# Kernel tuning notes

Measured on AMD Instinct MI355X. Metric: run time of the kernel, lower is better.

Reference implementation:

```python
import jax, jax.numpy as jnp
import numpy as np

D = 256        # d_model
NH = 8         # num_head
NL = 4         # num_level
KS = 8         # kernel_size (even)
K2 = KS * KS
HD = D // NH   # head_dim
LEVELS = [(128, 128), (64, 64), (32, 32), (16, 16)]


def _kernel_indices():
    # even kernel: linspace(-KS/2+0.5, KS/2-0.5, KS), meshgrid ij, stack [j,i] (x,y), / KS
    idx = np.linspace(-KS // 2 + 0.5, KS // 2 - 0.5, KS).astype(np.float32)
    i, j = np.meshgrid(idx, idx, indexing='ij')
    return jnp.asarray(np.stack([j, i], axis=-1).reshape(-1, 2) / KS)  # [K2, 2]


def setup_inputs():
    key = jax.random.key(0)
    ks = jax.random.split(key, 12)
    b, q = 2, 300
    l2 = sum(h * w for h, w in LEVELS)
    query = jax.random.normal(ks[0], (b, q, D), jnp.float32)
    value = jax.random.normal(ks[1], (b, l2, D), jnp.float32)
    v_shape = np.array(LEVELS, dtype=np.int64)                      # [NL, 2] (H, W)
    starts = np.concatenate([[0], np.cumsum([h * w for h, w in LEVELS])[:-1]])
    v_start_index = starts.astype(np.int64)                          # [NL]
    v_mask = jnp.zeros((b, l2), dtype=bool)                          # no padding
    v_valid_ratios = jnp.ones((b, 1, 1, NL, 1, 2), jnp.float32)
    center = jax.random.uniform(ks[2], (b, q, 2), jnp.float32, 0.25, 0.75)
    size = jax.random.uniform(ks[3], (b, q, 2), jnp.float32, 0.05, 0.25)
    ref_windows = jnp.concatenate([center, size], axis=-1)           # [b, q, 4] cx,cy,w,h
    s = 0.02
    Wv = s * jax.random.normal(ks[4], (D, D), jnp.float32)
    bv = jnp.zeros((D,), jnp.float32)
    Wbox = s * jax.random.normal(ks[5], (NH * NL * 4, D), jnp.float32)
    bbox = jax.random.uniform(ks[6], (NH * NL * 4,), jnp.float32)    # uniform init per _reset_parameters
    Wattn = s * jax.random.normal(ks[7], (NH * NL * 4, D), jnp.float32)
    battn = s * jax.random.normal(ks[8], (NH * NL * 4,), jnp.float32)
    Wout = s * jax.random.normal(ks[9], (D, D), jnp.float32)
    bout = jnp.zeros((D,), jnp.float32)
    return dict(query=query, value=value, v_shape=v_shape, v_mask=v_mask,
                v_start_index=v_start_index, v_valid_ratios=v_valid_ratios,
                ref_windows=ref_windows, Wv=Wv, bv=bv, Wbox=Wbox, bbox=bbox,
                Wattn=Wattn, battn=battn, Wout=Wout, bout=bout,
                kernel_indices=_kernel_indices())


def reference(query, value, v_shape, v_mask, v_start_index, v_valid_ratios,
              ref_windows, Wv, bv, Wbox, bbox, Wattn, battn, Wout, bout,
              kernel_indices):
    b, q, _ = query.shape
    # value projection + mask fill
    val = jnp.einsum('bnd,ed->bne', value, Wv) + bv
    val = jnp.where(v_mask[..., None], 0.0, val)
    val = val.reshape(b, -1, NH, HD)                                 # [b, l2, NH, HD]

    # attention logits: base 2x2 grid expanded to KSxKS via repeat_interleave
    aw = (jnp.einsum('bqd,od->bqo', query, Wattn) + battn).reshape(b, q, NH, NL, 2, 2)
    aw = jnp.repeat(jnp.repeat(aw, KS // 2, axis=-1), KS // 2, axis=-2)  # [b,q,NH,NL,KS,KS]
    spatial = jax.nn.softmax(aw.reshape(b, q, NH, NL * K2), axis=-1).reshape(b, q, NH, NL, K2)
    level = jax.nn.softmax(aw, axis=3).reshape(b, q, NH, NL, K2)

    # sampling grid (_where_to_attend)
    ob = (jnp.einsum('bqd,od->bqo', query, Wbox) + bbox).reshape(b, q, NH, NL, 4)
    rw = ref_windows[:, :, None, None, :]                            # [b,q,1,1,4]
    boxes = rw + ob / 8.0 * rw[..., jnp.array([2, 3, 2, 3])]
    center = boxes[..., None, :2]                                    # [b,q,NH,NL,1,2]
    size = boxes[..., None, 2:]
    grid = center + kernel_indices * jax.nn.relu(size)               # [b,q,NH,NL,K2,2]
    grid = grid * v_valid_ratios

    # multi-level bilinear sampling (grid_sample, align_corners=False, zero padding)
    bi = jnp.arange(b)[:, None, None, None]
    hi = jnp.arange(NH)[None, None, :, None]
    sampled = []
    for lv in range(NL):
        Hl = int(v_shape[lv, 0]); Wl = int(v_shape[lv, 1]); st = int(v_start_index[lv])
        vl = val[:, st:st + Hl * Wl]                                 # [b, Hl*Wl, NH, HD]
        loc = grid[:, :, :, lv]                                      # [b,q,NH,K2,2]
        x = loc[..., 0] * Wl - 0.5
        y = loc[..., 1] * Hl - 0.5
        x0 = jnp.floor(x); y0 = jnp.floor(y)
        dx = x - x0; dy = y - y0
        acc = jnp.zeros((b, q, NH, K2, HD), val.dtype)
        for ix, iy, w in ((x0, y0, (1 - dx) * (1 - dy)),
                          (x0 + 1, y0, dx * (1 - dy)),
                          (x0, y0 + 1, (1 - dx) * dy),
                          (x0 + 1, y0 + 1, dx * dy)):
            valid = (ix >= 0) & (ix < Wl) & (iy >= 0) & (iy < Hl)
            idx = (jnp.clip(iy, 0, Hl - 1) * Wl + jnp.clip(ix, 0, Wl - 1)).astype(jnp.int32)
            v4 = vl[bi, idx, hi]                                     # [b,q,NH,K2,HD]
            acc = acc + jnp.where(valid, w, 0.0)[..., None] * v4
        sampled.append(acc)
    sampled = jnp.stack(sampled, axis=3)                             # [b,q,NH,NL,K2,HD]

    # box-attention output: spatial softmax over all (level, point)
    out = jnp.einsum('bqhlkd,bqhlk->bqhd', sampled, spatial).reshape(b, q, D)
    out = jnp.einsum('bqd,od->bqo', out, Wout) + bout
    # instance mask output: level softmax per kernel point
    mask = jnp.einsum('bqhlkd,bqhlk->bqkhd', sampled, level).reshape(b, q, K2, D)
    mask = jnp.einsum('bqkd,od->bqko', mask, Wout) + bout
    return out, mask
```

## Files before the change

### kernel.cpp

```cpp
#include <hip/hip_runtime.h>
#include <cstdint>
#include <cstddef>

typedef unsigned short u16;
typedef unsigned int   u32;
typedef __attribute__((ext_vector_type(8))) short bf16x8;
typedef __attribute__((ext_vector_type(4))) float f32x4;

static constexpr int kQ = 300;
static constexpr int kL2 = 21760;

__device__ __forceinline__ u16 bf16_rne(float f) {
    u32 u = __float_as_uint(f);
    u += 0x7FFFu + ((u >> 16) & 1u);
    return (u16)(u >> 16);
}
__device__ __forceinline__ u32 pack2(float lo, float hi) {
    return (u32)bf16_rne(lo) | ((u32)bf16_rne(hi) << 16);
}
__device__ __forceinline__ float lo16(u32 u) { return __uint_as_float(u << 16); }
__device__ __forceinline__ float hi16(u32 u) { return __uint_as_float(u & 0xFFFF0000u); }

#define GLOAD(kt) { \
    const int k0 = (kt) * 32; \
    if constexpr (A_F32) { \
        const float* p = (const float*)Aptr + (size_t)(m0 + arow) * 256 + k0 + asub * 8; \
        ra0 = *(const float4*)p; ra1 = *(const float4*)(p + 4); \
    } else { \
        rav = *(const uint4*)((const u16*)Aptr + (size_t)(m0 + arow) * 256 + k0 + asub * 8); \
    } \
    rb0 = *(const uint4*)(W + (size_t)(n0 + b0row) * 256 + k0 + bsub * 8); \
    rb1 = *(const uint4*)(W + (size_t)(n0 + b1row) * 256 + k0 + bsub * 8); }

#define GSTORE(buf) { \
    u16* As = S + (buf) * 6144; \
    u16* Bs = As + 2048; \
    const int ac = asub * 64 + ((arow + 2 * asub) & 63); \
    if constexpr (A_F32) { \
        uint4 o; \
        o.x = pack2(ra0.x, ra0.y); o.y = pack2(ra0.z, ra0.w); \
        o.z = pack2(ra1.x, ra1.y); o.w = pack2(ra1.z, ra1.w); \
        *(uint4*)(As + (ac << 3)) = o; \
    } else { \
        *(uint4*)(As + (ac << 3)) = rav; \
    } \
    *(uint4*)(Bs + ((bsub * 128 + ((b0row + 2 * bsub) & 127)) << 3)) = rb0; \
    *(uint4*)(Bs + ((bsub * 128 + ((b1row + 2 * bsub) & 127)) << 3)) = rb1; }

template<bool A_F32, bool OUT_BF16>
__global__ __launch_bounds__(256)
void gemm_bf16(const void* __restrict__ Aptr, const u16* __restrict__ W,
               const float* __restrict__ bias, void* __restrict__ Cout,
               const unsigned char* __restrict__ rowmask)
{
    __shared__ u16 S[12288];
    const int tid = threadIdx.x;
    const int m0 = blockIdx.x * 64;
    const int n0 = blockIdx.y * 128;
    const int lane = tid & 63;
    const int w = tid >> 6;
    const int wm = w & 1, wn = w >> 1;
    const int g = lane >> 4, r = lane & 15;

    const int arow = tid >> 2, asub = tid & 3;
    const int b0row = tid >> 2;
    const int b1row = 64 + (tid >> 2);
    const int bsub = tid & 3;

    f32x4 acc[2][4];
#pragma unroll
    for (int i = 0; i < 2; i++)
#pragma unroll
        for (int j = 0; j < 4; j++)
            acc[i][j] = (f32x4){0.f, 0.f, 0.f, 0.f};

    float4 ra0, ra1; uint4 rav; uint4 rb0, rb1;

    GLOAD(0);
    GSTORE(0);
    for (int kt = 0; kt < 8; ++kt) {
        if (kt < 7) GLOAD(kt + 1);
        __syncthreads();
        const u16* As = S + (kt & 1) * 6144;
        const u16* Bs = As + 2048;
        bf16x8 af[2], bf[4];
#pragma unroll
        for (int mf = 0; mf < 2; ++mf) {
            int X = wm * 32 + mf * 16 + r;
            af[mf] = *(const bf16x8*)(As + ((g * 64 + ((X + 2 * g) & 63)) << 3));
        }
#pragma unroll
        for (int nf = 0; nf < 4; ++nf) {
            int X = wn * 64 + nf * 16 + r;
            bf[nf] = *(const bf16x8*)(Bs + ((g * 128 + ((X + 2 * g) & 127)) << 3));
        }
#pragma unroll
        for (int mf = 0; mf < 2; ++mf)
#pragma unroll
            for (int nf = 0; nf < 4; ++nf)
                acc[mf][nf] = __builtin_amdgcn_mfma_f32_16x16x32_bf16(
                    af[mf], bf[nf], acc[mf][nf], 0, 0, 0);
        if (kt < 7) GSTORE((kt + 1) & 1);
    }

    if constexpr (!OUT_BF16) {
        float* C = (float*)Cout;
#pragma unroll
        for (int nf = 0; nf < 4; ++nf) {
            int ng = n0 + wn * 64 + nf * 16 + r;
            float bb = bias[ng];
#pragma unroll
            for (int mf = 0; mf < 2; ++mf) {
                int mg = m0 + wm * 32 + mf * 16 + g * 4;
#pragma unroll
                for (int reg = 0; reg < 4; ++reg) {
                    float z = 1.f;
                    if (rowmask && rowmask[mg + reg]) z = 0.f;
                    C[(size_t)(mg + reg) * 256 + ng] = (acc[mf][nf][reg] + bb) * z;
                }
            }
        }
    } else {
        u16* C = (u16*)Cout;
#pragma unroll
        for (int round = 0; round < 2; ++round) {
            __syncthreads();
            if (wn == round) {
#pragma unroll
                for (int nf = 0; nf < 4; ++nf) {
                    int col = nf * 16 + r;
                    float bb = bias[n0 + round * 64 + col];
#pragma unroll
                    for (int mf = 0; mf < 2; ++mf) {
                        int row0 = wm * 32 + mf * 16 + g * 4;
#pragma unroll
                        for (int reg = 0; reg < 4; ++reg) {
                            float z = 1.f;
                            if (rowmask && rowmask[m0 + row0 + reg]) z = 0.f;
                            S[(row0 + reg) * 64 + col] =
                                bf16_rne((acc[mf][nf][reg] + bb) * z);
                        }
                    }
                }
            }
            __syncthreads();
#pragma unroll
            for (int i = 0; i < 2; ++i) {
                int c = tid + i * 256;
                int row = c >> 3, cc = c & 7;
                *(uint4*)(C + (size_t)(m0 + row) * 256 + n0 + round * 64 + cc * 8) =
                    *(const uint4*)(S + row * 64 + cc * 8);
            }
        }
    }
}

__global__ __launch_bounds__(256)
void gemm_out_fused(const float* __restrict__ out_part, const float* __restrict__ W,
                    const float* __restrict__ bias, float* __restrict__ C, int M)
{
    __shared__ float As[32][68];
    __shared__ float Ws[32][68];
    const int tid = threadIdx.x;
    const int m0 = blockIdx.x * 64;
    const int n0 = blockIdx.y * 64;
    const int tx = tid & 15, ty = tid >> 4;
    const size_t KQS = (size_t)600 * 256;
    float acc[4][4] = {};

    for (int k0 = 0; k0 < 256; k0 += 32) {
#pragma unroll
        for (int i = 0; i < 2; i++) {
            int t = tid + i * 256;
            int rr = t >> 3;
            int c4 = (t & 7) << 2;
            int ra = min(m0 + rr, M - 1);
            const float* p = out_part + (size_t)ra * 256 + k0 + c4;
            float4 v0 = *(const float4*)p;
            float4 v1 = *(const float4*)(p + KQS);
            float4 v2 = *(const float4*)(p + 2 * KQS);
            float4 v3 = *(const float4*)(p + 3 * KQS);
            float4 va;
            va.x = (v0.x + v1.x) + (v2.x + v3.x);
            va.y = (v0.y + v1.y) + (v2.y + v3.y);
            va.z = (v0.z + v1.z) + (v2.z + v3.z);
            va.w = (v0.w + v1.w) + (v2.w + v3.w);
            As[c4 + 0][rr] = va.x; As[c4 + 1][rr] = va.y;
            As[c4 + 2][rr] = va.z; As[c4 + 3][rr] = va.w;
            float4 vw = *(const float4*)(W + (size_t)(n0 + rr) * 256 + k0 + c4);
            Ws[c4 + 0][rr] = vw.x; Ws[c4 + 1][rr] = vw.y;
            Ws[c4 + 2][rr] = vw.z; Ws[c4 + 3][rr] = vw.w;
        }
        __syncthreads();
#pragma unroll
        for (int kk = 0; kk < 32; kk++) {
            float4 a = *(const float4*)&As[kk][ty * 4];
            float4 wv4 = *(const float4*)&Ws[kk][tx * 4];
            float av[4] = {a.x, a.y, a.z, a.w};
            float wv[4] = {wv4.x, wv4.y, wv4.z, wv4.w};
#pragma unroll
            for (int i = 0; i < 4; i++)
#pragma unroll
                for (int j = 0; j < 4; j++)
                    acc[i][j] += av[i] * wv[j];
        }
        __syncthreads();
    }
#pragma unroll
    for (int i = 0; i < 4; i++) {
        int rr = m0 + ty * 4 + i;
        if (rr >= M) continue;
        int n = n0 + tx * 4;
        float4 o;
        o.x = acc[i][0] + bias[n + 0];
        o.y = acc[i][1] + bias[n + 1];
        o.z = acc[i][2] + bias[n + 2];
        o.w = acc[i][3] + bias[n + 3];
        *(float4*)(C + (size_t)rr * 256 + n) = o;
    }
}

__global__ __launch_bounds__(256)
void prep_kernel(const float* __restrict__ Wv, u16* __restrict__ Wv_b,
                 const float* __restrict__ Wout, u16* __restrict__ Wout_b,
                 const float* __restrict__ query,
                 const float* __restrict__ Wattn, const float* __restrict__ battn,
                 const float* __restrict__ Wbox,  const float* __restrict__ bbox,
                 const float* __restrict__ ref_windows,
                 const float* __restrict__ vvr,
                 float* __restrict__ params)
{
    if (blockIdx.x < 64) {
        const float* src = (blockIdx.x < 32) ? Wv : Wout;
        u16* dst = (blockIdx.x < 32) ? Wv_b : Wout_b;
        int i = ((blockIdx.x & 31) * 256 + threadIdx.x) * 8;
        float4 a = *(const float4*)(src + i);
        float4 b = *(const float4*)(src + i + 4);
        uint4 o;
        o.x = pack2(a.x, a.y); o.y = pack2(a.z, a.w);
        o.z = pack2(b.x, b.y); o.w = pack2(b.z, b.w);
        *(uint4*)(dst + i) = o;
        return;
    }

    __shared__ float qrow[256];
    __shared__ float awob[256];
    __shared__ float4 boxs[8][4];
    __shared__ float wgts[8][4][4];
    __shared__ float cqds[8][4];

    const int bq = blockIdx.x - 64;
    const int b = bq / kQ;
    const int tid = threadIdx.x;

    if (tid < 64)
        ((float4*)qrow)[tid] = ((const float4*)(query + (size_t)bq * 256))[tid];
    __syncthreads();

    {
        const float* Wrow = (tid < 128) ? (Wattn + (size_t)tid * 256)
                                        : (Wbox + (size_t)(tid - 128) * 256);
        float s = (tid < 128) ? battn[tid] : bbox[tid - 128];
#pragma unroll 8
        for (int d4 = 0; d4 < 64; d4++) {
            float4 wv = ((const float4*)Wrow)[d4];
            float4 qv = ((const float4*)qrow)[d4];
            s += wv.x * qv.x + wv.y * qv.y + wv.z * qv.z + wv.w * qv.w;
        }
        awob[tid] = s;
    }
    __syncthreads();

    if (tid < 8) {
        const int h = tid;
        float m = -1e30f;
        float E[16];
#pragma unroll
        for (int i = 0; i < 16; i++) m = fmaxf(m, awob[h * 16 + i]);
        float Ssum = 0.f;
#pragma unroll
        for (int i = 0; i < 16; i++) { E[i] = expf(awob[h * 16 + i] - m); Ssum += E[i]; }
        float invS16 = 1.f / (16.f * Ssum);
#pragma unroll
        for (int qd = 0; qd < 4; qd++) {
            float Sq = E[qd] + E[4 + qd] + E[8 + qd] + E[12 + qd];
            float inv = 1.f / Sq;
#pragma unroll
            for (int l = 0; l < 4; l++) wgts[h][l][qd] = E[l * 4 + qd] * inv;
            cqds[h][qd] = Sq * invS16;
        }
    }
    if (tid >= 64 && tid < 96) {
        const int t = tid - 64;
        const int h = t >> 2, l = t & 3;
        float4 rw = ((const float4*)ref_windows)[bq];
        float ob0 = awob[128 + h * 16 + l * 4 + 0];
        float ob1 = awob[128 + h * 16 + l * 4 + 1];
        float ob2 = awob[128 + h * 16 + l * 4 + 2];
        float ob3 = awob[128 + h * 16 + l * 4 + 3];
        float cx = rw.x + ob0 * 0.125f * rw.z;
        float cy = rw.y + ob1 * 0.125f * rw.w;
        float sx = fmaxf(rw.z + ob2 * 0.125f * rw.z, 0.f);
        float sy = fmaxf(rw.w + ob3 * 0.125f * rw.w, 0.f);
        float vrx = vvr[(b * 4 + l) * 2 + 0];
        float vry = vvr[(b * 4 + l) * 2 + 1];
        boxs[h][l] = make_float4(cx * vrx, cy * vry, sx * vrx, sy * vry);
    }
    __syncthreads();

    float* p = params + (size_t)bq * 288;
    if (tid < 32)       ((float4*)p)[tid] = ((float4*)boxs)[tid];
    else if (tid < 64)  ((float4*)p)[tid] = ((float4*)wgts)[tid - 32];
    else if (tid < 72)  ((float4*)p)[tid] = ((float4*)cqds)[tid - 64];
}

__global__ __launch_bounds__(512)
void sample_bf16(const u16* __restrict__ valb,
                 const float* __restrict__ params,
                 u16* __restrict__ maskb,
                 float* __restrict__ out_part)
{
    __shared__ float4 boxs[8][4];
    __shared__ float wgts[8][4][4];
    __shared__ float cqds[8][4];
    __shared__ float warr[8][256];

    const int blk = blockIdx.x;
    const int bq = blk % 600;
    const int kq = blk / 600;
    const int b = bq / kQ;
    const int tid = threadIdx.x;

    if (tid < 72) {
        float4 v = ((const float4*)(params + (size_t)bq * 288))[tid];
        if (tid < 32)      ((float4*)boxs)[tid] = v;
        else if (tid < 64) ((float4*)wgts)[tid - 32] = v;
        else               ((float4*)cqds)[tid - 64] = v;
    }
    __syncthreads();

    const int klocal = tid >> 5;
    const int h = (tid >> 2) & 7;
    const int ch = tid & 3;
    const int k = kq * 16 + klocal;
    const float kx = (float)(k & 7) * 0.125f - 0.4375f;
    const float ky = (float)(k >> 3) * 0.125f - 0.4375f;
    const int qd = (((k >> 5) & 1) << 1) | ((k >> 2) & 1);

    float acc[8];
#pragma unroll
    for (int e = 0; e < 8; e++) acc[e] = 0.f;

    static constexpr int LW[4]  = {128, 64, 32, 16};
    static constexpr int LST[4] = {0, 16384, 20480, 21504};

#pragma unroll
    for (int l = 0; l < 4; l++) {
        const int Wl = LW[l];
        const u16* vbase = valb + ((size_t)(b * kL2 + LST[l]) << 8) + h * 32 + ch * 8;
        float4 bx = boxs[h][l];
        float lw = wgts[h][l][qd];
        float x = (bx.x + kx * bx.z) * Wl - 0.5f;
        float y = (bx.y + ky * bx.w) * Wl - 0.5f;
        float x0f = floorf(x), y0f = floorf(y);
        float dx = x - x0f, dy = y - y0f;
        int x0 = (int)x0f, y0 = (int)y0f;
        int x1 = x0 + 1, y1 = y0 + 1;
        int x0c = min(max(x0, 0), Wl - 1), x1c = min(max(x1, 0), Wl - 1);
        int y0c = min(max(y0, 0), Wl - 1), y1c = min(max(y1, 0), Wl - 1);
        float vx0 = (x0 >= 0 && x0 < Wl) ? 1.f : 0.f;
        float vx1 = (x1 >= 0 && x1 < Wl) ? 1.f : 0.f;
        float vy0 = (y0 >= 0 && y0 < Wl) ? 1.f : 0.f;
        float vy1 = (y1 >= 0 && y1 < Wl) ? 1.f : 0.f;
        float w00 = (1.f - dx) * (1.f - dy) * vx0 * vy0 * lw;
        float w10 = dx * (1.f - dy) * vx1 * vy0 * lw;
        float w01 = (1.f - dx) * dy * vx0 * vy1 * lw;
        float w11 = dx * dy * vx1 * vy1 * lw;
        uint4 v00 = *(const uint4*)(vbase + ((size_t)(y0c * Wl + x0c) << 8));
        uint4 v10 = *(const uint4*)(vbase + ((size_t)(y0c * Wl + x1c) << 8));
        uint4 v01 = *(const uint4*)(vbase + ((size_t)(y1c * Wl + x0c) << 8));
        uint4 v11 = *(const uint4*)(vbase + ((size_t)(y1c * Wl + x1c) << 8));
        acc[0] += w00*lo16(v00.x) + w10*lo16(v10.x) + w01*lo16(v01.x) + w11*lo16(v11.x);
        acc[1] += w00*hi16(v00.x) + w10*hi16(v10.x) + w01*hi16(v01.x) + w11*hi16(v11.x);
        acc[2] += w00*lo16(v00.y) + w10*lo16(v10.y) + w01*lo16(v01.y) + w11*lo16(v11.y);
        acc[3] += w00*hi16(v00.y) + w10*hi16(v10.y) + w01*hi16(v01.y) + w11*hi16(v11.y);
        acc[4] += w00*lo16(v00.z) + w10*lo16(v10.z) + w01*lo16(v01.z) + w11*lo16(v11.z);
        acc[5] += w00*hi16(v00.z) + w10*hi16(v10.z) + w01*hi16(v01.z) + w11*hi16(v11.z);
        acc[6] += w00*lo16(v00.w) + w10*lo16(v10.w) + w01*lo16(v01.w) + w11*lo16(v11.w);
        acc[7] += w00*hi16(v00.w) + w10*hi16(v10.w) + w01*hi16(v01.w) + w11*hi16(v11.w);
    }

    {
        uint4 o;
        o.x = pack2(acc[0], acc[1]);
        o.y = pack2(acc[2], acc[3]);
        o.z = pack2(acc[4], acc[5]);
        o.w = pack2(acc[6], acc[7]);
        *(uint4*)(maskb + (((size_t)bq * 64 + k) << 8) + h * 32 + ch * 8) = o;
    }

    {
        const int wave = tid >> 6;
        const int lane = tid & 63;
        float c = cqds[h][qd];
#pragma unroll
        for (int e = 0; e < 8; e++) {
            float v = acc[e] * c;
            v += __shfl_xor(v, 32);
            if (lane < 32) warr[wave][h * 32 + ch * 8 + e] = v;
        }
    }
    __syncthreads();
    if (tid < 256) {
        float s = 0.f;
#pragma unroll
        for (int wv = 0; wv < 8; wv++) s += warr[wv][tid];
        out_part[(size_t)blk * 256 + tid] = s;
    }
}

extern "C" void kernel_launch(void* const* d_in, const int* in_sizes, int n_in,
                              void* d_out, int out_size, void* d_ws, size_t ws_size,
                              hipStream_t stream)
{
    const float* query       = (const float*)d_in[0];
    const float* value       = (const float*)d_in[1];
    const unsigned char* v_mask = (const unsigned char*)d_in[3];
    const float* vvr         = (const float*)d_in[5];
    const float* ref_windows = (const float*)d_in[6];
    const float* Wv    = (const float*)d_in[7];
    const float* bv    = (const float*)d_in[8];
    const float* Wbox  = (const float*)d_in[9];
    const float* bbox  = (const float*)d_in[10];
    const float* Wattn = (const float*)d_in[11];
    const float* battn = (const float*)d_in[12];
    const float* Wout  = (const float*)d_in[13];
    const float* bout  = (const float*)d_in[14];

    char* wsp = (char*)d_ws;
    u16* Wv_b    = (u16*)wsp;                 wsp += (size_t)65536 * 2;
    u16* Wout_b  = (u16*)wsp;                 wsp += (size_t)65536 * 2;
    u16* val_b   = (u16*)wsp;                 wsp += (size_t)11141120 * 2;
    u16* mask_b  = (u16*)wsp;                 wsp += (size_t)9830400 * 2;
    float* params   = (float*)wsp;            wsp += (size_t)600 * 288 * 4;
    float* out_part = (float*)wsp;            wsp += (size_t)2400 * 256 * 4;

    float* out  = (float*)d_out;
    float* mask = out + (size_t)600 * 256;

    prep_kernel<<<664, 256, 0, stream>>>(Wv, Wv_b, Wout, Wout_b,
                                         query, Wattn, battn, Wbox, bbox,
                                         ref_windows, vvr, params);
    gemm_bf16<true, true><<<dim3(680, 2), 256, 0, stream>>>(value, Wv_b, bv, val_b, v_mask);
    sample_bf16<<<2400, 512, 0, stream>>>(val_b, params, mask_b, out_part);
    gemm_bf16<false, false><<<dim3(600, 2), 256, 0, stream>>>(mask_b, Wout_b, bout, mask, nullptr);
    gemm_out_fused<<<dim3(10, 4), 256, 0, stream>>>(out_part, Wout, bout, out, 600);
}
```

Baseline: 127.3 us.

## Process two kernel points per thread in sampler and merge output GEMM into mask GEMM

Each sampling thread now handles two horizontally adjacent kernel points. They share the y interpolation and row bases, which halves the sampler grid and the number of partial-output slices. The small fp32 output projection no longer has its own launch: it runs as 20 extra blocks of the mask GEMM grid, and it sums two partial slices instead of four. Occupancy hints are also added to the sampler. The intent is to cut launch overhead and redundant coordinate math, at the cost of more registers per thread and fewer sampler blocks.

```diff
diff --git a/kernel.cpp b/kernel.cpp
--- a/kernel.cpp
+++ b/kernel.cpp
@@ -47,14 +47,79 @@
     *(uint4*)(Bs + ((bsub * 128 + ((b0row + 2 * bsub) & 127)) << 3)) = rb0; \
     *(uint4*)(Bs + ((bsub * 128 + ((b1row + 2 * bsub) & 127)) << 3)) = rb1; }
 
-template<bool A_F32, bool OUT_BF16>
+template<bool A_F32, bool OUT_BF16, bool MERGED_OUT>
 __global__ __launch_bounds__(256)
 void gemm_bf16(const void* __restrict__ Aptr, const u16* __restrict__ W,
                const float* __restrict__ bias, void* __restrict__ Cout,
-               const unsigned char* __restrict__ rowmask)
+               const unsigned char* __restrict__ rowmask,
+               const float* __restrict__ Wf,
+               const float* __restrict__ opart,
+               float* __restrict__ C2)
 {
     __shared__ u16 S[12288];
     const int tid = threadIdx.x;
+
+    if constexpr (MERGED_OUT) {
+        if (blockIdx.x >= 600) {
+            float (*As2)[68] = reinterpret_cast<float(*)[68]>(S);
+            float (*Ws2)[68] = reinterpret_cast<float(*)[68]>((char*)S + 8704);
+            const int t20 = blockIdx.x - 600;
+            const int m0o = (t20 % 10) * 64;
+            const int nq  = (t20 / 10) * 2 + blockIdx.y;
+            const int n0o = nq * 64;
+            const int tx = tid & 15, ty = tid >> 4;
+            const size_t KQS = (size_t)600 * 256;
+            float acc[4][4] = {};
+            for (int k0 = 0; k0 < 256; k0 += 32) {
+#pragma unroll
+                for (int i = 0; i < 2; i++) {
+                    int t = tid + i * 256;
+                    int rr = t >> 3;
+                    int c4 = (t & 7) << 2;
+                    int ra = min(m0o + rr, 599);
+                    const float* p = opart + (size_t)ra * 256 + k0 + c4;
+                    float4 v0 = *(const float4*)p;
+                    float4 v1 = *(const float4*)(p + KQS);
+                    float4 va;
+                    va.x = v0.x + v1.x; va.y = v0.y + v1.y;
+                    va.z = v0.z + v1.z; va.w = v0.w + v1.w;
+                    As2[c4 + 0][rr] = va.x; As2[c4 + 1][rr] = va.y;
+                    As2[c4 + 2][rr] = va.z; As2[c4 + 3][rr] = va.w;
+                    float4 vw = *(const float4*)(Wf + (size_t)(n0o + rr) * 256 + k0 + c4);
+                    Ws2[c4 + 0][rr] = vw.x; Ws2[c4 + 1][rr] = vw.y;
+                    Ws2[c4 + 2][rr] = vw.z; Ws2[c4 + 3][rr] = vw.w;
+                }
+                __syncthreads();
+#pragma unroll
+                for (int kk = 0; kk < 32; kk++) {
+                    float4 a = *(const float4*)&As2[kk][ty * 4];
+                    float4 wv4 = *(const float4*)&Ws2[kk][tx * 4];
+                    float av[4] = {a.x, a.y, a.z, a.w};
+                    float wv[4] = {wv4.x, wv4.y, wv4.z, wv4.w};
+#pragma unroll
+                    for (int i = 0; i < 4; i++)
+#pragma unroll
+                        for (int jj = 0; jj < 4; jj++)
+                            acc[i][jj] += av[i] * wv[jj];
+                }
+                __syncthreads();
+            }
+#pragma unroll
+            for (int i = 0; i < 4; i++) {
+                int rr = m0o + ty * 4 + i;
+                if (rr >= 600) continue;
+                int n = n0o + tx * 4;
+                float4 o;
+                o.x = acc[i][0] + bias[n + 0];
+                o.y = acc[i][1] + bias[n + 1];
+                o.z = acc[i][2] + bias[n + 2];
+                o.w = acc[i][3] + bias[n + 3];
+                *(float4*)(C2 + (size_t)rr * 256 + n) = o;
+            }
+            return;
+        }
+    }
+
     const int m0 = blockIdx.x * 64;
     const int n0 = blockIdx.y * 128;
     const int lane = tid & 63;
@@ -152,71 +217,6 @@
                     *(const uint4*)(S + row * 64 + cc * 8);
             }
         }
-    }
-}
-
-__global__ __launch_bounds__(256)
-void gemm_out_fused(const float* __restrict__ out_part, const float* __restrict__ W,
-                    const float* __restrict__ bias, float* __restrict__ C, int M)
-{
-    __shared__ float As[32][68];
-    __shared__ float Ws[32][68];
-    const int tid = threadIdx.x;
-    const int m0 = blockIdx.x * 64;
-    const int n0 = blockIdx.y * 64;
-    const int tx = tid & 15, ty = tid >> 4;
-    const size_t KQS = (size_t)600 * 256;
-    float acc[4][4] = {};
-
-    for (int k0 = 0; k0 < 256; k0 += 32) {
-#pragma unroll
-        for (int i = 0; i < 2; i++) {
-            int t = tid + i * 256;
-            int rr = t >> 3;
-            int c4 = (t & 7) << 2;
-            int ra = min(m0 + rr, M - 1);
-            const float* p = out_part + (size_t)ra * 256 + k0 + c4;
-            float4 v0 = *(const float4*)p;
-            float4 v1 = *(const float4*)(p + KQS);
-            float4 v2 = *(const float4*)(p + 2 * KQS);
-            float4 v3 = *(const float4*)(p + 3 * KQS);
-            float4 va;
-            va.x = (v0.x + v1.x) + (v2.x + v3.x);
-            va.y = (v0.y + v1.y) + (v2.y + v3.y);
-            va.z = (v0.z + v1.z) + (v2.z + v3.z);
-            va.w = (v0.w + v1.w) + (v2.w + v3.w);
-            As[c4 + 0][rr] = va.x; As[c4 + 1][rr] = va.y;
-            As[c4 + 2][rr] = va.z; As[c4 + 3][rr] = va.w;
-            float4 vw = *(const float4*)(W + (size_t)(n0 + rr) * 256 + k0 + c4);
-            Ws[c4 + 0][rr] = vw.x; Ws[c4 + 1][rr] = vw.y;
-            Ws[c4 + 2][rr] = vw.z; Ws[c4 + 3][rr] = vw.w;
-        }
-        __syncthreads();
-#pragma unroll
-        for (int kk = 0; kk < 32; kk++) {
-            float4 a = *(const float4*)&As[kk][ty * 4];
-            float4 wv4 = *(const float4*)&Ws[kk][tx * 4];
-            float av[4] = {a.x, a.y, a.z, a.w};
-            float wv[4] = {wv4.x, wv4.y, wv4.z, wv4.w};
-#pragma unroll
-            for (int i = 0; i < 4; i++)
-#pragma unroll
-                for (int j = 0; j < 4; j++)
-                    acc[i][j] += av[i] * wv[j];
-        }
-        __syncthreads();
-    }
-#pragma unroll
-    for (int i = 0; i < 4; i++) {
-        int rr = m0 + ty * 4 + i;
-        if (rr >= M) continue;
-        int n = n0 + tx * 4;
-        float4 o;
-        o.x = acc[i][0] + bias[n + 0];
-        o.y = acc[i][1] + bias[n + 1];
-        o.z = acc[i][2] + bias[n + 2];
-        o.w = acc[i][3] + bias[n + 3];
-        *(float4*)(C + (size_t)rr * 256 + n) = o;
     }
 }
 
@@ -314,7 +314,7 @@
     else if (tid < 72)  ((float4*)p)[tid] = ((float4*)cqds)[tid - 64];
 }
 
-__global__ __launch_bounds__(512)
+__global__ __launch_bounds__(512, 4)
 void sample_bf16(const u16* __restrict__ valb,
                  const float* __restrict__ params,
                  u16* __restrict__ maskb,
@@ -327,7 +327,7 @@
 
     const int blk = blockIdx.x;
     const int bq = blk % 600;
-    const int kq = blk / 600;
+    const int kh = blk / 600;
     const int b = bq / kQ;
     const int tid = threadIdx.x;
 
@@ -339,17 +339,19 @@
     }
     __syncthreads();
 
-    const int klocal = tid >> 5;
+    const int j = tid >> 5;
     const int h = (tid >> 2) & 7;
     const int ch = tid & 3;
-    const int k = kq * 16 + klocal;
-    const float kx = (float)(k & 7) * 0.125f - 0.4375f;
-    const float ky = (float)(k >> 3) * 0.125f - 0.4375f;
-    const int qd = (((k >> 5) & 1) << 1) | ((k >> 2) & 1);
-
-    float acc[8];
-#pragma unroll
-    for (int e = 0; e < 8; e++) acc[e] = 0.f;
+    const int J = kh * 16 + j;
+    const int ka = 2 * J;
+    const float kxa = (float)(ka & 7) * 0.125f - 0.4375f;
+    const float kxb = kxa + 0.125f;
+    const float ky  = (float)(ka >> 3) * 0.125f - 0.4375f;
+    const int qd = (((ka >> 5) & 1) << 1) | ((ka >> 2) & 1);
+
+    float acca[8], accb[8];
+#pragma unroll
+    for (int e = 0; e < 8; e++) { acca[e] = 0.f; accb[e] = 0.f; }
 
     static constexpr int LW[4]  = {128, 64, 32, 16};
     static constexpr int LST[4] = {0, 16384, 20480, 21504};
@@ -360,43 +362,56 @@
         const u16* vbase = valb + ((size_t)(b * kL2 + LST[l]) << 8) + h * 32 + ch * 8;
         float4 bx = boxs[h][l];
         float lw = wgts[h][l][qd];
-        float x = (bx.x + kx * bx.z) * Wl - 0.5f;
         float y = (bx.y + ky * bx.w) * Wl - 0.5f;
-        float x0f = floorf(x), y0f = floorf(y);
-        float dx = x - x0f, dy = y - y0f;
-        int x0 = (int)x0f, y0 = (int)y0f;
-        int x1 = x0 + 1, y1 = y0 + 1;
-        int x0c = min(max(x0, 0), Wl - 1), x1c = min(max(x1, 0), Wl - 1);
+        float y0f = floorf(y);
+        float dy = y - y0f;
+        int y0 = (int)y0f, y1 = y0 + 1;
         int y0c = min(max(y0, 0), Wl - 1), y1c = min(max(y1, 0), Wl - 1);
-        float vx0 = (x0 >= 0 && x0 < Wl) ? 1.f : 0.f;
-        float vx1 = (x1 >= 0 && x1 < Wl) ? 1.f : 0.f;
         float vy0 = (y0 >= 0 && y0 < Wl) ? 1.f : 0.f;
         float vy1 = (y1 >= 0 && y1 < Wl) ? 1.f : 0.f;
-        float w00 = (1.f - dx) * (1.f - dy) * vx0 * vy0 * lw;
-        float w10 = dx * (1.f - dy) * vx1 * vy0 * lw;
-        float w01 = (1.f - dx) * dy * vx0 * vy1 * lw;
-        float w11 = dx * dy * vx1 * vy1 * lw;
-        uint4 v00 = *(const uint4*)(vbase + ((size_t)(y0c * Wl + x0c) << 8));
-        uint4 v10 = *(const uint4*)(vbase + ((size_t)(y0c * Wl + x1c) << 8));
-        uint4 v01 = *(const uint4*)(vbase + ((size_t)(y1c * Wl + x0c) << 8));
-        uint4 v11 = *(const uint4*)(vbase + ((size_t)(y1c * Wl + x1c) << 8));
-        acc[0] += w00*lo16(v00.x) + w10*lo16(v10.x) + w01*lo16(v01.x) + w11*lo16(v11.x);
-        acc[1] += w00*hi16(v00.x) + w10*hi16(v10.x) + w01*hi16(v01.x) + w11*hi16(v11.x);
-        acc[2] += w00*lo16(v00.y) + w10*lo16(v10.y) + w01*lo16(v01.y) + w11*lo16(v11.y);
-        acc[3] += w00*hi16(v00.y) + w10*hi16(v10.y) + w01*hi16(v01.y) + w11*hi16(v11.y);
-        acc[4] += w00*lo16(v00.z) + w10*lo16(v10.z) + w01*lo16(v01.z) + w11*lo16(v11.z);
-        acc[5] += w00*hi16(v00.z) + w10*hi16(v10.z) + w01*hi16(v01.z) + w11*hi16(v11.z);
-        acc[6] += w00*lo16(v00.w) + w10*lo16(v10.w) + w01*lo16(v01.w) + w11*lo16(v11.w);
-        acc[7] += w00*hi16(v00.w) + w10*hi16(v10.w) + w01*hi16(v01.w) + w11*hi16(v11.w);
+        float wy0 = (1.f - dy) * vy0 * lw;
+        float wy1 = dy * vy1 * lw;
+        const u16* rbase0 = vbase + ((size_t)(y0c * Wl) << 8);
+        const u16* rbase1 = vbase + ((size_t)(y1c * Wl) << 8);
+#pragma unroll
+        for (int s = 0; s < 2; ++s) {
+            float kx = s ? kxb : kxa;
+            float* acc = s ? accb : acca;
+            float x = (bx.x + kx * bx.z) * Wl - 0.5f;
+            float x0f = floorf(x);
+            float dx = x - x0f;
+            int x0 = (int)x0f, x1 = x0 + 1;
+            int x0c = min(max(x0, 0), Wl - 1), x1c = min(max(x1, 0), Wl - 1);
+            float vx0 = (x0 >= 0 && x0 < Wl) ? 1.f : 0.f;
+            float vx1 = (x1 >= 0 && x1 < Wl) ? 1.f : 0.f;
+            float w00 = (1.f - dx) * vx0 * wy0;
+            float w10 = dx * vx1 * wy0;
+            float w01 = (1.f - dx) * vx0 * wy1;
+            float w11 = dx * vx1 * wy1;
+            uint4 v00 = *(const uint4*)(rbase0 + ((size_t)x0c << 8));
+            uint4 v10 = *(const uint4*)(rbase0 + ((size_t)x1c << 8));
+            uint4 v01 = *(const uint4*)(rbase1 + ((size_t)x0c << 8));
+            uint4 v11 = *(const uint4*)(rbase1 + ((size_t)x1c << 8));
+            acc[0] += w00*lo16(v00.x) + w10*lo16(v10.x) + w01*lo16(v01.x) + w11*lo16(v11.x);
+            acc[1] += w00*hi16(v00.x) + w10*hi16(v10.x) + w01*hi16(v01.x) + w11*hi16(v11.x);
+            acc[2] += w00*lo16(v00.y) + w10*lo16(v10.y) + w01*lo16(v01.y) + w11*lo16(v11.y);
+            acc[3] += w00*hi16(v00.y) + w10*hi16(v10.y) + w01*hi16(v01.y) + w11*hi16(v11.y);
+            acc[4] += w00*lo16(v00.z) + w10*lo16(v10.z) + w01*lo16(v01.z) + w11*lo16(v11.z);
+            acc[5] += w00*hi16(v00.z) + w10*hi16(v10.z) + w01*hi16(v01.z) + w11*hi16(v11.z);
+            acc[6] += w00*lo16(v00.w) + w10*lo16(v10.w) + w01*lo16(v01.w) + w11*lo16(v11.w);
+            acc[7] += w00*hi16(v00.w) + w10*hi16(v10.w) + w01*hi16(v01.w) + w11*hi16(v11.w);
+        }
     }
 
     {
-        uint4 o;
-        o.x = pack2(acc[0], acc[1]);
-        o.y = pack2(acc[2], acc[3]);
-        o.z = pack2(acc[4], acc[5]);
-        o.w = pack2(acc[6], acc[7]);
-        *(uint4*)(maskb + (((size_t)bq * 64 + k) << 8) + h * 32 + ch * 8) = o;
+        uint4 oa, ob;
+        oa.x = pack2(acca[0], acca[1]); oa.y = pack2(acca[2], acca[3]);
+        oa.z = pack2(acca[4], acca[5]); oa.w = pack2(acca[6], acca[7]);
+        ob.x = pack2(accb[0], accb[1]); ob.y = pack2(accb[2], accb[3]);
+        ob.z = pack2(accb[4], accb[5]); ob.w = pack2(accb[6], accb[7]);
+        u16* mrow = maskb + (((size_t)bq * 64 + ka) << 8) + h * 32 + ch * 8;
+        *(uint4*)mrow = oa;
+        *(uint4*)(mrow + 256) = ob;
     }
 
     {
@@ -405,7 +420,7 @@
         float c = cqds[h][qd];
 #pragma unroll
         for (int e = 0; e < 8; e++) {
-            float v = acc[e] * c;
+            float v = (acca[e] + accb[e]) * c;
             v += __shfl_xor(v, 32);
             if (lane < 32) warr[wave][h * 32 + ch * 8 + e] = v;
         }
@@ -443,7 +458,7 @@
     u16* val_b   = (u16*)wsp;                 wsp += (size_t)11141120 * 2;
     u16* mask_b  = (u16*)wsp;                 wsp += (size_t)9830400 * 2;
     float* params   = (float*)wsp;            wsp += (size_t)600 * 288 * 4;
-    float* out_part = (float*)wsp;            wsp += (size_t)2400 * 256 * 4;
+    float* out_part = (float*)wsp;            wsp += (size_t)1200 * 256 * 4;
 
     float* out  = (float*)d_out;
     float* mask = out + (size_t)600 * 256;
@@ -451,8 +466,9 @@
     prep_kernel<<<664, 256, 0, stream>>>(Wv, Wv_b, Wout, Wout_b,
                                          query, Wattn, battn, Wbox, bbox,
                                          ref_windows, vvr, params);
-    gemm_bf16<true, true><<<dim3(680, 2), 256, 0, stream>>>(value, Wv_b, bv, val_b, v_mask);
-    sample_bf16<<<2400, 512, 0, stream>>>(val_b, params, mask_b, out_part);
-    gemm_bf16<false, false><<<dim3(600, 2), 256, 0, stream>>>(mask_b, Wout_b, bout, mask, nullptr);
-    gemm_out_fused<<<dim3(10, 4), 256, 0, stream>>>(out_part, Wout, bout, out, 600);
-}
+    gemm_bf16<true, true, false><<<dim3(680, 2), 256, 0, stream>>>(
+        value, Wv_b, bv, val_b, v_mask, nullptr, nullptr, nullptr);
+    sample_bf16<<<1200, 512, 0, stream>>>(val_b, params, mask_b, out_part);
+    gemm_bf16<false, false, true><<<dim3(620, 2), 256, 0, stream>>>(
+        mask_b, Wout_b, bout, mask, nullptr, Wout, out_part, out);
+}
```

After: 227.5 us. +78.7%, slower.
